# Kernel tuning notes

Measured on AMD Instinct MI355X. Metric: run time of the kernel, lower is better.

The kernel has to match this reference:

```python
import jax, jax.numpy as jnp
import numpy as np

IN_F = 256
OUT_F = 256
HYPER = 128
BATCH = 4096


def setup_inputs() -> dict:
    key = jax.random.key(0)
    ks = jax.random.split(key, 9)
    s_in = 1.0 / np.sqrt(IN_F)
    s_h = 1.0 / np.sqrt(HYPER)
    x = jax.random.normal(ks[0], (BATCH, IN_F), dtype=jnp.float32)
    # weight_gen: Linear(in, hyper) -> ReLU -> Linear(hyper, in*out)
    W1g = jax.random.uniform(ks[1], (IN_F, HYPER), jnp.float32, -s_in, s_in)
    b1g = jax.random.uniform(ks[2], (HYPER,), jnp.float32, -s_in, s_in)
    W2g = jax.random.uniform(ks[3], (HYPER, IN_F * OUT_F), jnp.float32, -s_h, s_h)
    b2g = jax.random.uniform(ks[4], (IN_F * OUT_F,), jnp.float32, -s_h, s_h)
    # bias_gen: Linear(in, hyper) -> ReLU -> Linear(hyper, out)
    W1b = jax.random.uniform(ks[5], (IN_F, HYPER), jnp.float32, -s_in, s_in)
    b1b = jax.random.uniform(ks[6], (HYPER,), jnp.float32, -s_in, s_in)
    W2b = jax.random.uniform(ks[7], (HYPER, OUT_F), jnp.float32, -s_h, s_h)
    b2b = jax.random.uniform(ks[8], (OUT_F,), jnp.float32, -s_h, s_h)
    return {"x": x, "W1g": W1g, "b1g": b1g, "W2g": W2g, "b2g": b2g,
            "W1b": W1b, "b1b": b1b, "W2b": W2b, "b2b": b2b}


def reference(x, W1g, b1g, W2g, b2g, W1b, b1b, W2b, b2b):
    B = x.shape[0]
    # generate per-sample weights [B, out, in]
    hg = jax.nn.relu(x @ W1g + b1g)                      # [B, hyper]
    weights = (hg @ W2g + b2g).reshape(B, OUT_F, IN_F)   # [B, out, in]
    # generate per-sample bias [B, out]
    hb = jax.nn.relu(x @ W1b + b1b)                      # [B, hyper]
    bias = hb @ W2b + b2b                                # [B, out]
    # batched matvec: bmm(weights, x[...,None]) + bias
    out = jnp.einsum('boi,bi->bo', weights, x) + bias    # [B, out]
    return out
```

## Files before the change

kernel.cpp:

```cpp
#include <hip/hip_runtime.h>

#define AS1 __attribute__((address_space(1)))
#define AS3 __attribute__((address_space(3)))

typedef short short8 __attribute__((ext_vector_type(8)));
typedef float f32x16 __attribute__((ext_vector_type(16)));
typedef unsigned short ushort4v __attribute__((ext_vector_type(4)));

#define BATCH 4096
#define IN_F 256
#define OUT_F 256
#define HYP 128
#define HX 129
#define KP (HX * IN_F)
#define NGEMMP 32
#define NVB 516

__device__ __forceinline__ float bf2f(unsigned short u) {
  unsigned v = ((unsigned)u) << 16;
  float f;
  __builtin_memcpy(&f, &v, 4);
  return f;
}
__device__ __forceinline__ unsigned short f2bf(float f) {
  unsigned u;
  __builtin_memcpy(&u, &f, 4);
  unsigned r = u + 0x7fffu + ((u >> 16) & 1u);
  return (unsigned short)(r >> 16);
}

__device__ __forceinline__ void gld_lds16(const unsigned short* g, unsigned short* s) {
  __builtin_amdgcn_global_load_lds((const AS1 unsigned int*)g, (AS3 unsigned int*)s, 16, 0, 0);
}

__global__ __launch_bounds__(256) void k_trans(const float* __restrict__ W1g,
                                               const float* __restrict__ W1b,
                                               const float* __restrict__ W2b,
                                               unsigned short* __restrict__ W1T,
                                               unsigned short* __restrict__ W2bT) {
  const int t = threadIdx.x, b = blockIdx.x;
  if (b < 64) {
#pragma unroll
    for (int i = 0; i < 4; ++i) {
      const int e = b * 1024 + i * 256 + t;
      const int n = e >> 8, k = e & 255;
      const float v = (n < HYP) ? W1g[k * HYP + n] : W1b[k * HYP + (n - HYP)];
      W1T[e] = f2bf(v);
    }
  } else {
#pragma unroll
    for (int i = 0; i < 4; ++i) {
      const int e = (b - 64) * 1024 + i * 256 + t;
      const int o = e >> 7, h = e & 127;
      W2bT[e] = f2bf(W2b[h * OUT_F + o]);
    }
  }
}

__global__ __launch_bounds__(512) void k_prep(
    const float* __restrict__ x,
    const float* __restrict__ b1g, const float* __restrict__ b1b,
    const float* __restrict__ b2b,
    const float* __restrict__ W2g, const float* __restrict__ b2g,
    const unsigned short* __restrict__ W1T, const unsigned short* __restrict__ W2bT,
    unsigned short* __restrict__ Vb, unsigned short* __restrict__ hgbT,
    unsigned short* __restrict__ xb, float* __restrict__ out) {
  __shared__ __align__(16) unsigned short xS[128 * 256];
  __shared__ __align__(16) unsigned short hbS[128 * 128];
  const int t = threadIdx.x;

  if (blockIdx.x >= NGEMMP) {
    const int base = (blockIdx.x - NGEMMP) * 2048 + t;
#pragma unroll
    for (int it = 0; it < 4; ++it) {
      const int cid = base + it * 512;
      const int ic = cid & 31;
      const int pair = cid >> 5;
      const int h = pair % HX;
      const int o = pair / HX;
      const float* src = (h < HYP) ? (W2g + (size_t)h * (OUT_F * IN_F) + o * IN_F + ic * 8)
                                   : (b2g + o * IN_F + ic * 8);
      const float4 v0 = ((const float4*)src)[0];
      const float4 v1 = ((const float4*)src)[1];
      uint4 pk;
      pk.x = (unsigned)f2bf(v0.x) | ((unsigned)f2bf(v0.y) << 16);
      pk.y = (unsigned)f2bf(v0.z) | ((unsigned)f2bf(v0.w) << 16);
      pk.z = (unsigned)f2bf(v1.x) | ((unsigned)f2bf(v1.y) << 16);
      pk.w = (unsigned)f2bf(v1.z) | ((unsigned)f2bf(v1.w) << 16);
      *(uint4*)(Vb + (size_t)o * KP + h * IN_F + ic * 8) = pk;
    }
    return;
  }

  const int lane = t & 63;
  const int w = t >> 6;
  const int l31 = lane & 31;
  const int hi = lane >> 5;
  const int m0 = blockIdx.x * 128;

#pragma unroll
  for (int j = 0; j < 16; ++j) {
    const int row = j * 8 + w;
    const float4 v = *(const float4*)(x + (size_t)(m0 + row) * IN_F + lane * 4);
    uint2 pk;
    pk.x = (unsigned)f2bf(v.x) | ((unsigned)f2bf(v.y) << 16);
    pk.y = (unsigned)f2bf(v.z) | ((unsigned)f2bf(v.w) << 16);
    *(uint2*)(xb + (size_t)(m0 + row) * IN_F + lane * 4) = pk;
    const int ch = lane >> 1, half = lane & 1;
    *(uint2*)(&xS[row * 256 + ((ch ^ (row & 31))) * 8 + half * 4]) = pk;
  }
  __syncthreads();

  const int hA = w * 32 + l31;
  uint4 af[16];
#pragma unroll
  for (int kt = 0; kt < 16; ++kt)
    af[kt] = *(const uint4*)(W1T + (size_t)hA * 256 + kt * 16 + hi * 8);

  f32x16 zv;
#pragma unroll
  for (int i = 0; i < 16; ++i) zv[i] = 0.0f;
  f32x16 d0 = zv, d1 = zv, d2 = zv, d3 = zv;
#pragma unroll
  for (int kt = 0; kt < 16; ++kt) {
    const int pos = (kt * 2 + hi) ^ l31;
    const short8 a = __builtin_bit_cast(short8, af[kt]);
#define G1STEP(CS, DD)                                                        \
    {                                                                         \
      const short8 bfrg = *(const short8*)(&xS[(CS * 32 + l31) * 256 + pos * 8]); \
      DD = __builtin_amdgcn_mfma_f32_32x32x16_bf16(a, bfrg, DD, 0, 0, 0);     \
    }
    G1STEP(0, d0) G1STEP(1, d1) G1STEP(2, d2) G1STEP(3, d3)
#undef G1STEP
  }

  if (w < 4) {
    float4 bq[4];
#pragma unroll
    for (int q = 0; q < 4; ++q)
      bq[q] = *(const float4*)(b1g + w * 32 + q * 8 + hi * 4);
#define EPI_G(CS, DD)                                                         \
    {                                                                         \
      const int mcol = m0 + CS * 32 + l31;                                    \
      _Pragma("unroll")                                                       \
      for (int g = 0; g < 16; ++g) {                                          \
        const int h = w * 32 + (g & 3) + 8 * (g >> 2) + 4 * hi;               \
        float v = DD[g] + ((const float*)&bq[g >> 2])[g & 3];                 \
        v = v > 0.f ? v : 0.f;                                                \
        hgbT[(size_t)h * BATCH + mcol] = f2bf(v);                             \
      }                                                                       \
    }
    EPI_G(0, d0) EPI_G(1, d1) EPI_G(2, d2) EPI_G(3, d3)
#undef EPI_G
  } else {
    float4 bq[4];
#pragma unroll
    for (int q = 0; q < 4; ++q)
      bq[q] = *(const float4*)(b1b + (w - 4) * 32 + q * 8 + hi * 4);
#define EPI_B(CS, DD)                                                         \
    {                                                                         \
      const int m = CS * 32 + l31;                                            \
      _Pragma("unroll")                                                       \
      for (int q = 0; q < 4; ++q) {                                           \
        float v0 = DD[q * 4 + 0] + ((const float*)&bq[q])[0];                 \
        float v1 = DD[q * 4 + 1] + ((const float*)&bq[q])[1];                 \
        float v2 = DD[q * 4 + 2] + ((const float*)&bq[q])[2];                 \
        float v3 = DD[q * 4 + 3] + ((const float*)&bq[q])[3];                 \
        v0 = v0 > 0.f ? v0 : 0.f; v1 = v1 > 0.f ? v1 : 0.f;                   \
        v2 = v2 > 0.f ? v2 : 0.f; v3 = v3 > 0.f ? v3 : 0.f;                   \
        uint2 pk;                                                             \
        pk.x = (unsigned)f2bf(v0) | ((unsigned)f2bf(v1) << 16);               \
        pk.y = (unsigned)f2bf(v2) | ((unsigned)f2bf(v3) << 16);               \
        const int chunk = (w - 4) * 4 + q;                                    \
        *(uint2*)(&hbS[m * 128 + ((chunk ^ (m & 15))) * 8 + hi * 4]) = pk;    \
      }                                                                       \
    }
    EPI_B(0, d0) EPI_B(1, d1) EPI_B(2, d2) EPI_B(3, d3)
#undef EPI_B
  }
  __syncthreads();

  const int msub = w & 3, oh = w >> 2;
  const int mA = msub * 32 + l31;
  f32x16 e0 = zv, e1 = zv, e2 = zv, e3 = zv;
#pragma unroll
  for (int kt = 0; kt < 8; ++kt) {
    const int pos = (kt * 2 + hi) ^ (mA & 15);
    const short8 a = *(const short8*)(&hbS[mA * 128 + pos * 8]);
#define G2STEP(OS, EE)                                                        \
    {                                                                         \
      const int orow = oh * 128 + OS * 32 + l31;                              \
      const short8 bb = *(const short8*)(W2bT + (size_t)orow * 128 + kt * 16 + hi * 8); \
      EE = __builtin_amdgcn_mfma_f32_32x32x16_bf16(a, bb, EE, 0, 0, 0);       \
    }
    G2STEP(0, e0) G2STEP(1, e1) G2STEP(2, e2) G2STEP(3, e3)
#undef G2STEP
  }
#define EPI2(OS, EE)                                                          \
  {                                                                           \
    const int o = oh * 128 + OS * 32 + l31;                                   \
    const float bo = b2b[o];                                                  \
    _Pragma("unroll")                                                         \
    for (int g = 0; g < 16; ++g) {                                            \
      const int m = m0 + msub * 32 + (g & 3) + 8 * (g >> 2) + 4 * hi;         \
      out[(size_t)m * OUT_F + o] = EE[g] + bo;                                \
    }                                                                         \
  }
  EPI2(0, e0) EPI2(1, e1) EPI2(2, e2) EPI2(3, e3)
#undef EPI2
}

__global__ __launch_bounds__(512)
__attribute__((amdgpu_waves_per_eu(2, 2)))
void k_gemm(const unsigned short* __restrict__ Vb,
            const unsigned short* __restrict__ hgbT,
            const unsigned short* __restrict__ xb,
            float* __restrict__ out) {
  __shared__ __align__(16) unsigned short Bl[2][64 * 256];
  __shared__ __align__(16) unsigned short hgs[33 * 256];
  const int tid = threadIdx.x;
  const int lane = tid & 63;
  const int wave = tid >> 6;
  const int l31 = lane & 31;
  const int hi = lane >> 5;
  const int wm = wave & 3;
  const int wo = wave >> 2;

  const int bid = blockIdx.x;
  const int c = bid & 7;
  const int t2 = bid >> 3;
  const int xm = t2 & 15;
  const int g8 = t2 >> 4;
  const int grp = c + 8 * g8;
  const int yo = grp & 3;
  const int z = grp >> 2;

  const int m0 = xm * 256;
  const int o0 = yo * 64;
  const int hBeg = (z * HX) >> 2;
  const int hEnd = ((z + 1) * HX) >> 2;
  const int nh = hEnd - hBeg;

  for (int idx = tid; idx < nh * 256; idx += 512) {
    const int hl = idx >> 8;
    const int hh = hBeg + hl;
    hgs[idx] = (hh == HYP) ? (unsigned short)0x3F80
                           : hgbT[(size_t)hh * BATCH + m0 + (idx & 255)];
  }

  const int mrow0 = m0 + wm * 64 + l31;
  const int mrow1 = mrow0 + 32;
  uint4 xf0[16], xf1[16];
#pragma unroll
  for (int j = 0; j < 16; ++j) {
    xf0[j] = *(const uint4*)(xb + (size_t)mrow0 * IN_F + j * 16 + hi * 8);
    xf1[j] = *(const uint4*)(xb + (size_t)mrow1 * IN_F + j * 16 + hi * 8);
  }

  const int nB = tid >> 5;
  const int p = tid & 31;
  const int cs = p ^ (nB & 7);
  const unsigned short* gsrc = Vb + (size_t)(o0 + nB) * KP + cs * 8 + (size_t)hBeg * IN_F;

  f32x16 zv;
#pragma unroll
  for (int i = 0; i < 16; ++i) zv[i] = 0.0f;
  f32x16 acc0 = zv, acc1 = zv;
  f32x16 ah0 = zv, ah1 = zv;

#pragma unroll
  for (int j = 0; j < 4; ++j)
    gld_lds16(gsrc + (size_t)j * 16 * KP, &Bl[0][(tid + 512 * j) * 8]);
  __syncthreads();

  for (int r = 0; r < nh; ++r) {
    const int buf = r & 1;
    if (r + 1 < nh) {
      const unsigned short* gs = gsrc + (size_t)(r + 1) * IN_F;
#pragma unroll
      for (int j = 0; j < 4; ++j)
        gld_lds16(gs + (size_t)j * 16 * KP, &Bl[buf ^ 1][(tid + 512 * j) * 8]);
    }
    const unsigned short* bp = &Bl[buf][0];
    const int rowb = wo * 32 + l31;
#pragma unroll
    for (int ic = 0; ic < 4; ++ic) {
#pragma unroll
      for (int t = 0; t < 4; ++t) {
        const int c0 = ic * 8 + t * 2 + hi;
        const int pr = c0 ^ (l31 & 7);
        const short8 b0 = *(const short8*)(bp + rowb * 256 + pr * 8);
        const short8 a0 = __builtin_bit_cast(short8, xf0[ic * 4 + t]);
        const short8 a1 = __builtin_bit_cast(short8, xf1[ic * 4 + t]);
        ah0 = __builtin_amdgcn_mfma_f32_32x32x16_bf16(a0, b0, ah0, 0, 0, 0);
        ah1 = __builtin_amdgcn_mfma_f32_32x32x16_bf16(a1, b0, ah1, 0, 0, 0);
      }
    }
#pragma unroll
    for (int q = 0; q < 4; ++q) {
      const ushort4v v0 = *(const ushort4v*)&hgs[r * 256 + wm * 64 + 4 * hi + q * 8];
      const ushort4v v1 = *(const ushort4v*)&hgs[r * 256 + wm * 64 + 32 + 4 * hi + q * 8];
#pragma unroll
      for (int e = 0; e < 4; ++e) {
        acc0[q * 4 + e] += bf2f(v0[e]) * ah0[q * 4 + e];
        acc1[q * 4 + e] += bf2f(v1[e]) * ah1[q * 4 + e];
      }
    }
    ah0 = zv; ah1 = zv;
    __syncthreads();
  }

  const int mb = m0 + wm * 64 + 4 * hi;
  const int col = o0 + wo * 32 + l31;
#pragma unroll
  for (int g = 0; g < 16; ++g) {
    const int row0 = mb + (g & 3) + 8 * (g >> 2);
    atomicAdd(&out[(size_t)row0 * OUT_F + col], acc0[g]);
    atomicAdd(&out[(size_t)(row0 + 32) * OUT_F + col], acc1[g]);
  }
}

extern "C" void kernel_launch(void* const* d_in, const int* in_sizes, int n_in,
                              void* d_out, int out_size, void* d_ws, size_t ws_size,
                              hipStream_t stream) {
  const float* x = (const float*)d_in[0];
  const float* W1g = (const float*)d_in[1];
  const float* b1g = (const float*)d_in[2];
  const float* W2g = (const float*)d_in[3];
  const float* b2g = (const float*)d_in[4];
  const float* W1b = (const float*)d_in[5];
  const float* b1b = (const float*)d_in[6];
  const float* W2b = (const float*)d_in[7];
  const float* b2b = (const float*)d_in[8];
  float* out = (float*)d_out;

  char* ws = (char*)d_ws;
  const size_t szV = (size_t)OUT_F * KP * 2;
  const size_t szHg = (size_t)HYP * BATCH * 2;
  const size_t szXb = (size_t)BATCH * IN_F * 2;
  const size_t szW1T = (size_t)256 * 256 * 2;
  unsigned short* Vb = (unsigned short*)ws;
  unsigned short* hgbT = (unsigned short*)(ws + szV);
  unsigned short* xb = (unsigned short*)(ws + szV + szHg);
  unsigned short* W1T = (unsigned short*)(ws + szV + szHg + szXb);
  unsigned short* W2bT = (unsigned short*)(ws + szV + szHg + szXb + szW1T);

  hipLaunchKernelGGL(k_trans, dim3(96), dim3(256), 0, stream, W1g, W1b, W2b, W1T, W2bT);
  hipLaunchKernelGGL(k_prep, dim3(NGEMMP + NVB), dim3(512), 0, stream,
                     x, b1g, b1b, b2b, W2g, b2g, W1T, W2bT, Vb, hgbT, xb, out);
  hipLaunchKernelGGL(k_gemm, dim3(256), dim3(512), 0, stream, Vb, hgbT, xb, out);
}
```

Before: 189.5 us.

## Triple-buffer LDS weight stream with a single barrier and interleaved prefetch

Replaces the double-buffered LDS staging of the generated-weight tiles with a three-deep ring. Two stages are prefetched up front, hand-written vmcnt waits and one s_barrier per iteration replace the trailing __syncthreads, and the next-next stage's loads are interleaved with the MFMA groups. MFMA issue is raised with s_setprio. The hidden-activation tile is pre-converted to fp32 in LDS so the per-iteration bf16 unpacking goes away. The cost is noticeably more LDS per block and reliance on hand-counted waitcnt values being correct.

```diff
diff --git a/kernel.cpp b/kernel.cpp
--- a/kernel.cpp
+++ b/kernel.cpp
@@ -5,7 +5,6 @@
 
 typedef short short8 __attribute__((ext_vector_type(8)));
 typedef float f32x16 __attribute__((ext_vector_type(16)));
-typedef unsigned short ushort4v __attribute__((ext_vector_type(4)));
 
 #define BATCH 4096
 #define IN_F 256
@@ -210,14 +209,13 @@
 #undef EPI2
 }
 
-__global__ __launch_bounds__(512)
-__attribute__((amdgpu_waves_per_eu(2, 2)))
+__global__ __launch_bounds__(512, 2)
 void k_gemm(const unsigned short* __restrict__ Vb,
             const unsigned short* __restrict__ hgbT,
             const unsigned short* __restrict__ xb,
             float* __restrict__ out) {
-  __shared__ __align__(16) unsigned short Bl[2][64 * 256];
-  __shared__ __align__(16) unsigned short hgs[33 * 256];
+  __shared__ __align__(16) unsigned short Bl[3][64 * 256];
+  __shared__ __align__(16) float hgsF[33 * 256];
   const int tid = threadIdx.x;
   const int lane = tid & 63;
   const int wave = tid >> 6;
@@ -244,8 +242,8 @@
   for (int idx = tid; idx < nh * 256; idx += 512) {
     const int hl = idx >> 8;
     const int hh = hBeg + hl;
-    hgs[idx] = (hh == HYP) ? (unsigned short)0x3F80
-                           : hgbT[(size_t)hh * BATCH + m0 + (idx & 255)];
+    hgsF[idx] = (hh == HYP) ? 1.0f
+                            : bf2f(hgbT[(size_t)hh * BATCH + m0 + (idx & 255)]);
   }
 
   const int mrow0 = m0 + wm * 64 + l31;
@@ -258,8 +256,8 @@
   }
 
   const int nB = tid >> 5;
-  const int p = tid & 31;
-  const int cs = p ^ (nB & 7);
+  const int p5 = tid & 31;
+  const int cs = p5 ^ (nB & 7);
   const unsigned short* gsrc = Vb + (size_t)(o0 + nB) * KP + cs * 8 + (size_t)hBeg * IN_F;
 
   f32x16 zv;
@@ -270,44 +268,56 @@
 
 #pragma unroll
   for (int j = 0; j < 4; ++j)
-    gld_lds16(gsrc + (size_t)j * 16 * KP, &Bl[0][(tid + 512 * j) * 8]);
-  __syncthreads();
-
+    gld_lds16(gsrc + (size_t)j * 16 * KP, &Bl[0][((size_t)tid + 512 * j) * 8]);
+#pragma unroll
+  for (int j = 0; j < 4; ++j)
+    gld_lds16(gsrc + IN_F + (size_t)j * 16 * KP, &Bl[1][((size_t)tid + 512 * j) * 8]);
+  asm volatile("s_waitcnt lgkmcnt(0)" ::: "memory");
+
+  const int rowb = wo * 32 + l31;
   for (int r = 0; r < nh; ++r) {
-    const int buf = r & 1;
-    if (r + 1 < nh) {
-      const unsigned short* gs = gsrc + (size_t)(r + 1) * IN_F;
-#pragma unroll
-      for (int j = 0; j < 4; ++j)
-        gld_lds16(gs + (size_t)j * 16 * KP, &Bl[buf ^ 1][(tid + 512 * j) * 8]);
-    }
-    const unsigned short* bp = &Bl[buf][0];
-    const int rowb = wo * 32 + l31;
-#pragma unroll
-    for (int ic = 0; ic < 4; ++ic) {
-#pragma unroll
-      for (int t = 0; t < 4; ++t) {
-        const int c0 = ic * 8 + t * 2 + hi;
+    if (r + 1 < nh) asm volatile("s_waitcnt vmcnt(4)" ::: "memory");
+    else            asm volatile("s_waitcnt vmcnt(0)" ::: "memory");
+    asm volatile("s_barrier" ::: "memory");
+
+    const unsigned short* bp = &Bl[r % 3][0];
+    const bool issue = (r + 2 < nh);
+    unsigned short* nxt = &Bl[(r + 2) % 3][0];
+    const unsigned short* gs = gsrc + (size_t)(r + 2) * IN_F;
+
+#pragma unroll
+    for (int p = 0; p < 4; ++p) {
+      if (issue)
+        gld_lds16(gs + (size_t)p * 16 * KP, nxt + ((size_t)tid + 512 * p) * 8);
+      short8 bfr[4];
+#pragma unroll
+      for (int tt = 0; tt < 4; ++tt) {
+        const int c0 = p * 8 + tt * 2 + hi;
         const int pr = c0 ^ (l31 & 7);
-        const short8 b0 = *(const short8*)(bp + rowb * 256 + pr * 8);
-        const short8 a0 = __builtin_bit_cast(short8, xf0[ic * 4 + t]);
-        const short8 a1 = __builtin_bit_cast(short8, xf1[ic * 4 + t]);
-        ah0 = __builtin_amdgcn_mfma_f32_32x32x16_bf16(a0, b0, ah0, 0, 0, 0);
-        ah1 = __builtin_amdgcn_mfma_f32_32x32x16_bf16(a1, b0, ah1, 0, 0, 0);
+        bfr[tt] = *(const short8*)(bp + rowb * 256 + pr * 8);
       }
-    }
+      __builtin_amdgcn_s_setprio(1);
+#pragma unroll
+      for (int tt = 0; tt < 4; ++tt) {
+        const short8 a0 = __builtin_bit_cast(short8, xf0[p * 4 + tt]);
+        const short8 a1 = __builtin_bit_cast(short8, xf1[p * 4 + tt]);
+        ah0 = __builtin_amdgcn_mfma_f32_32x32x16_bf16(a0, bfr[tt], ah0, 0, 0, 0);
+        ah1 = __builtin_amdgcn_mfma_f32_32x32x16_bf16(a1, bfr[tt], ah1, 0, 0, 0);
+      }
+      __builtin_amdgcn_s_setprio(0);
+    }
+
 #pragma unroll
     for (int q = 0; q < 4; ++q) {
-      const ushort4v v0 = *(const ushort4v*)&hgs[r * 256 + wm * 64 + 4 * hi + q * 8];
-      const ushort4v v1 = *(const ushort4v*)&hgs[r * 256 + wm * 64 + 32 + 4 * hi + q * 8];
+      const float4 hv0 = *(const float4*)&hgsF[r * 256 + wm * 64 + 4 * hi + q * 8];
+      const float4 hv1 = *(const float4*)&hgsF[r * 256 + wm * 64 + 32 + 4 * hi + q * 8];
 #pragma unroll
       for (int e = 0; e < 4; ++e) {
-        acc0[q * 4 + e] += bf2f(v0[e]) * ah0[q * 4 + e];
-        acc1[q * 4 + e] += bf2f(v1[e]) * ah1[q * 4 + e];
+        acc0[q * 4 + e] += ((const float*)&hv0)[e] * ah0[q * 4 + e];
+        acc1[q * 4 + e] += ((const float*)&hv1)[e] * ah1[q * 4 + e];
       }
     }
     ah0 = zv; ah1 = zv;
-    __syncthreads();
   }
 
   const int mb = m0 + wm * 64 + 4 * hi;
```

New measurement: 198.9 us. 5.0% more time.
